# Kernel tuning notes

Hardware: AMD Instinct MI355X
Metric: run time of the kernel (lower is better)

## Reference

```python
import jax, jax.numpy as jnp
import numpy as np
import math

NHID = 8; NHEADS = 8; ALPHA = 0.2; EMB = 64  # nhid*nheads must equal selfattention embed_dim=64
NPROT = 2048; NDRUG = 1500; FPROT = 512; FDRUG = 256; NPAIR = 16384


def _layernorm(x, g, b):
    m = x.mean(-1, keepdims=True)
    v = ((x - m) ** 2).mean(-1, keepdims=True)
    return (x - m) / jnp.sqrt(v + 1e-5) * g + b


def _gat(h, adj, W, a):
    # W: [H,F,O], a: [H,2O].  e_ij = leakyrelu(Wh_i . a1 + Wh_j . a2)
    # (equivalent to the repeat_interleave/repeat/cat construction in the torch code)
    Wh = jnp.einsum('nf,hfo->hno', h, W)                 # [H,N,O]
    s1 = jnp.einsum('hno,ho->hn', Wh, a[:, :NHID])       # [H,N]
    s2 = jnp.einsum('hno,ho->hn', Wh, a[:, NHID:])       # [H,N]
    e = s1[:, :, None] + s2[:, None, :]                  # [H,N,N]
    e = jnp.where(e > 0, e, ALPHA * e)                   # LeakyReLU(alpha)
    e = jnp.where(adj[None, :, :] > 0, e, jnp.float32(-9e15))
    attn = jax.nn.softmax(e, axis=-1)
    out = jax.nn.relu(jnp.einsum('hnm,hmo->hno', attn, Wh))
    H, N, O = out.shape
    return out.transpose(1, 0, 2).reshape(N, H * O)      # concat heads along dim 1


def _mhsa_sum(x, W, b):
    # Sum of NHEADS independent selfattention(64, NHEADS) modules applied to x[None].
    # x: [N,EMB]; W: [3,M,EMB,EMB] torch (out,in) layout; b: [3,M,EMB]
    M = W.shape[1]; N = x.shape[0]; hd = EMB // NHEADS
    qkv = jnp.einsum('nd,smod->smno', x, W) + b[:, :, None, :]   # [3,M,N,EMB]
    q, k, v = [t.reshape(M, N, NHEADS, hd) for t in (qkv[0], qkv[1], qkv[2])]
    scores = jnp.einsum('mnhd,mkhd->mhnk', q, k) / math.sqrt(hd)
    attn = jax.nn.softmax(scores, axis=-1)
    out = jnp.einsum('mhnk,mkhd->mnhd', attn, v).reshape(M, N, EMB)
    return out.sum(0)


def _branch(h, adj, g1W, g1a, p1W, s1W, s1b, l1g, l1b, g2W, g2a, p2W, s2W, s2b, l2g, l2b):
    x = _gat(h, adj, g1W, g1a) @ p1W.T
    x = _layernorm(_mhsa_sum(x, s1W, s1b) + x, l1g, l1b)
    x = _gat(x, adj, g2W, g2a) @ p2W.T
    x = _layernorm(_mhsa_sum(x, s2W, s2b) + x, l2g, l2b)
    return x


def _forward(fl, idx):
    (pf, padj, df, dadj,
     pg1W, pg1a, pp1W, ps1W, ps1b, pl1g, pl1b, pg2W, pg2a, pp2W, ps2W, ps2b, pl2g, pl2b,
     dg1W, dg1a, dp1W, ds1W, ds1b, dl1g, dl1b, dg2W, dg2a, dp2W, ds2W, ds2b, dl2g, dl2b,
     fc1W, fc1b, fc2W, fc2b, fc3W, fc3b) = fl
    px = _branch(pf, padj, pg1W, pg1a, pp1W, ps1W, ps1b, pl1g, pl1b, pg2W, pg2a, pp2W, ps2W, ps2b, pl2g, pl2b)
    dx = _branch(df, dadj, dg1W, dg1a, dp1W, ds1W, ds1b, dl1g, dl1b, dg2W, dg2a, dp2W, ds2W, ds2b, dl2g, dl2b)
    x = jnp.concatenate([px[idx[:, 0]], dx[idx[:, 1]]], axis=1)   # [B, 2*EMB]
    x = jax.nn.relu(x @ fc1W.T + fc1b)
    x = jax.nn.relu(x @ fc2W.T + fc2b)
    return (x @ fc3W.T + fc3b)[:, 0]


def setup_inputs() -> dict:
    key = jax.random.key(0)
    ks = iter(jax.random.split(key, 80))
    nk = lambda: next(ks)
    rn = lambda shape, s=0.1: jax.random.normal(nk(), shape, jnp.float32) * s

    def adj(n):
        a = (jax.random.uniform(nk(), (n, n)) < 0.05).astype(jnp.float32)
        return jnp.maximum(a, jnp.eye(n, dtype=jnp.float32))

    inp = {}
    inp['protein_features'] = rn((NPROT, FPROT), 1.0)
    inp['protein_adj'] = adj(NPROT)
    inp['drug_features'] = rn((NDRUG, FDRUG), 1.0)
    inp['drug_adj'] = adj(NDRUG)
    ip = jax.random.randint(nk(), (NPAIR,), 0, NPROT)
    idd = jax.random.randint(nk(), (NPAIR,), 0, NDRUG)
    inp['idx_protein_drug'] = jnp.stack([ip, idd], axis=1).astype(jnp.int32)
    for pref, F in (('p', FPROT), ('d', FDRUG)):
        inp[pref + '_gat1_W'] = rn((NHEADS, F, NHID))
        inp[pref + '_gat1_a'] = rn((NHEADS, 2 * NHID))
        inp[pref + '_pro1_W'] = rn((EMB, EMB))
        inp[pref + '_sa1_W'] = rn((3, NHEADS, EMB, EMB))
        inp[pref + '_sa1_b'] = jnp.zeros((3, NHEADS, EMB), jnp.float32)
        inp[pref + '_ln1_g'] = jnp.ones((EMB,), jnp.float32)
        inp[pref + '_ln1_b'] = jnp.zeros((EMB,), jnp.float32)
        inp[pref + '_gat2_W'] = rn((NHEADS, EMB, NHID))
        inp[pref + '_gat2_a'] = rn((NHEADS, 2 * NHID))
        inp[pref + '_pro2_W'] = rn((EMB, EMB))
        inp[pref + '_sa2_W'] = rn((3, NHEADS, EMB, EMB))
        inp[pref + '_sa2_b'] = jnp.zeros((3, NHEADS, EMB), jnp.float32)
        inp[pref + '_ln2_g'] = jnp.ones((EMB,), jnp.float32)
        inp[pref + '_ln2_b'] = jnp.zeros((EMB,), jnp.float32)
    inp['fc1_W'] = rn((2 * EMB, 2 * EMB)); inp['fc1_b'] = jnp.zeros((2 * EMB,), jnp.float32)
    inp['fc2_W'] = rn((2 * EMB, 2 * EMB)); inp['fc2_b'] = jnp.zeros((2 * EMB,), jnp.float32)
    inp['fc3_W'] = rn((1, 2 * EMB)); inp['fc3_b'] = jnp.zeros((1,), jnp.float32)
    return inp


def reference(protein_features, protein_adj, drug_features, drug_adj, idx_protein_drug,
              p_gat1_W, p_gat1_a, p_pro1_W, p_sa1_W, p_sa1_b, p_ln1_g, p_ln1_b,
              p_gat2_W, p_gat2_a, p_pro2_W, p_sa2_W, p_sa2_b, p_ln2_g, p_ln2_b,
              d_gat1_W, d_gat1_a, d_pro1_W, d_sa1_W, d_sa1_b, d_ln1_g, d_ln1_b,
              d_gat2_W, d_gat2_a, d_pro2_W, d_sa2_W, d_sa2_b, d_ln2_g, d_ln2_b,
              fc1_W, fc1_b, fc2_W, fc2_b, fc3_W, fc3_b):
    fl = (protein_features, protein_adj, drug_features, drug_adj,
          p_gat1_W, p_gat1_a, p_pro1_W, p_sa1_W, p_sa1_b, p_ln1_g, p_ln1_b,
          p_gat2_W, p_gat2_a, p_pro2_W, p_sa2_W, p_sa2_b, p_ln2_g, p_ln2_b,
          d_gat1_W, d_gat1_a, d_pro1_W, d_sa1_W, d_sa1_b, d_ln1_g, d_ln1_b,
          d_gat2_W, d_gat2_a, d_pro2_W, d_sa2_W, d_sa2_b, d_ln2_g, d_ln2_b,
          fc1_W, fc1_b, fc2_W, fc2_b, fc3_W, fc3_b)
    return _forward(fl, idx_protein_drug)
```

## Files before the change

### kernel.cpp

```cpp
#include <hip/hip_runtime.h>
#include <math.h>

#define NHID 8
#define NHEADS 8
#define EMB 64
#define NPROT 2048
#define NDRUG 1500
#define NPAIR 16384

__global__ void k_gat_wh(const float* __restrict__ h, const float* __restrict__ W,
                         float* __restrict__ Wh, int N, int F) {
    int idx = blockIdx.x * 256 + threadIdx.x;
    int total = NHEADS * N * NHID;
    if (idx >= total) return;
    int o  = idx & 7;
    int n  = (idx >> 3) % N;
    int hh = idx / (N * 8);
    const float* hp = h + (size_t)n * F;
    const float* wp = W + (size_t)hh * F * 8 + o;
    float acc = 0.f;
    for (int f = 0; f < F; ++f) acc += hp[f] * wp[(size_t)f * 8];
    Wh[idx] = acc;
}

__global__ void k_gat_s(const float* __restrict__ Wh, const float* __restrict__ a,
                        float* __restrict__ s1, float* __restrict__ s2, int N) {
    int idx = blockIdx.x * 256 + threadIdx.x;
    if (idx >= NHEADS * N) return;
    int hh = idx / N;
    const float* wp = Wh + (size_t)idx * 8;
    const float* ap = a + hh * 16;
    float x1 = 0.f, x2 = 0.f;
    for (int o = 0; o < 8; ++o) { x1 += wp[o] * ap[o]; x2 += wp[o] * ap[8 + o]; }
    s1[idx] = x1; s2[idx] = x2;
}

__global__ void k_gat_attn(const float* __restrict__ adj, const float* __restrict__ s1,
                           const float* __restrict__ s2, const float* __restrict__ Wh,
                           float* __restrict__ out, int N) {
    __shared__ int nbr[2048];
    __shared__ int s_cnt;
    int i = blockIdx.x;
    int tid = threadIdx.x;
    if (tid == 0) s_cnt = 0;
    __syncthreads();
    const float* arow = adj + (size_t)i * N;
    for (int j = tid; j < N; j += 256)
        if (arow[j] > 0.f) { int p = atomicAdd(&s_cnt, 1); nbr[p] = j; }
    __syncthreads();
    int cnt = s_cnt;
    int g  = tid >> 5;
    int ln = tid & 31;
    float si = s1[g * N + i];
    const float* s2h = s2 + g * N;
    float mx = -1e30f;
    for (int t = ln; t < cnt; t += 32) {
        float e = si + s2h[nbr[t]];
        e = e > 0.f ? e : 0.2f * e;
        mx = fmaxf(mx, e);
    }
    #pragma unroll
    for (int off = 16; off; off >>= 1) mx = fmaxf(mx, __shfl_xor(mx, off, 32));
    float acc[8] = {0, 0, 0, 0, 0, 0, 0, 0};
    float lsum = 0.f;
    for (int t = ln; t < cnt; t += 32) {
        int j = nbr[t];
        float e = si + s2h[j];
        e = e > 0.f ? e : 0.2f * e;
        float p = __expf(e - mx);
        lsum += p;
        const float4* wp = (const float4*)(Wh + ((size_t)g * N + j) * 8);
        float4 w0 = wp[0], w1 = wp[1];
        acc[0] += p * w0.x; acc[1] += p * w0.y; acc[2] += p * w0.z; acc[3] += p * w0.w;
        acc[4] += p * w1.x; acc[5] += p * w1.y; acc[6] += p * w1.z; acc[7] += p * w1.w;
    }
    #pragma unroll
    for (int off = 16; off; off >>= 1) {
        lsum += __shfl_xor(lsum, off, 32);
        #pragma unroll
        for (int d = 0; d < 8; ++d) acc[d] += __shfl_xor(acc[d], off, 32);
    }
    if (ln == 0) {
        float inv = 1.f / lsum;
        #pragma unroll
        for (int d = 0; d < 8; ++d) {
            float r = acc[d] * inv;
            out[(size_t)i * 64 + g * 8 + d] = r > 0.f ? r : 0.f;
        }
    }
}

__global__ void k_proj(const float* __restrict__ in, const float* __restrict__ W,
                       float* __restrict__ out, int N) {
    int idx = blockIdx.x * 256 + threadIdx.x;
    if (idx >= N * 64) return;
    int o = idx & 63, n = idx >> 6;
    const float* ip = in + (size_t)n * 64;
    const float* wp = W + (size_t)o * 64;
    float acc = 0.f;
    for (int d = 0; d < 64; ++d) acc += ip[d] * wp[d];
    out[idx] = acc;
}

__global__ void k_qkv(const float* __restrict__ x, const float* __restrict__ W,
                      const float* __restrict__ b, float* __restrict__ qkv, int N) {
    int idx = blockIdx.x * 256 + threadIdx.x;
    int total = 24 * N * 64;
    if (idx >= total) return;
    int o = idx & 63;
    int n = (idx >> 6) % N;
    int sm = idx / (N * 64);
    const float* xp = x + (size_t)n * 64;
    const float* wp = W + ((size_t)sm * 64 + o) * 64;
    float acc = b[sm * 64 + o];
    for (int d = 0; d < 64; ++d) acc += xp[d] * wp[d];
    qkv[(size_t)sm * N * 64 + (size_t)(o >> 3) * N * 8 + (size_t)n * 8 + (o & 7)] = acc;
}

#define QLOAD(qa, qb, r) { int row_ = row0 + (r); if (row_ >= N) row_ = 0;        \
    const float4* qp_ = (const float4*)(qsl + (size_t)row_ * 8);                  \
    qa = qp_[0]; qb = qp_[1];                                                     \
    qa.x *= qs; qa.y *= qs; qa.z *= qs; qa.w *= qs;                               \
    qb.x *= qs; qb.y *= qs; qb.z *= qs; qb.w *= qs; }

#define ROWSTEP(qa, qb, ca, cb, lr) {                                             \
    float s_ = fmaf(qa.x, kk0.x, fmaf(qa.y, kk0.y, fmaf(qa.z, kk0.z,              \
               fmaf(qa.w, kk0.w, fmaf(qb.x, kk1.x, fmaf(qb.y, kk1.y,              \
               fmaf(qb.z, kk1.z, qb.w * kk1.w)))))));                             \
    float p_ = exp2f(s_); lr += p_;                                               \
    ca.x = fmaf(p_, vv0.x, ca.x); ca.y = fmaf(p_, vv0.y, ca.y);                   \
    ca.z = fmaf(p_, vv0.z, ca.z); ca.w = fmaf(p_, vv0.w, ca.w);                   \
    cb.x = fmaf(p_, vv1.x, cb.x); cb.y = fmaf(p_, vv1.y, cb.y);                   \
    cb.z = fmaf(p_, vv1.z, cb.z); cb.w = fmaf(p_, vv1.w, cb.w); }

#define BF3A(v) { v += __shfl_xor(v, 1, 64); v += __shfl_xor(v, 2, 64);           \
                  v += __shfl_xor(v, 4, 64); }

#define ROWOUT(ca, cb, lr, r) {                                                   \
    BF3A(ca.x); BF3A(ca.y); BF3A(ca.z); BF3A(ca.w);                               \
    BF3A(cb.x); BF3A(cb.y); BF3A(cb.z); BF3A(cb.w); BF3A(lr);                     \
    int sel_ = ln & 7;                                                            \
    float t_ = (sel_ == 0) ? ca.x : (sel_ == 1) ? ca.y : (sel_ == 2) ? ca.z :     \
               (sel_ == 3) ? ca.w : (sel_ == 4) ? cb.x : (sel_ == 5) ? cb.y :     \
               (sel_ == 6) ? cb.z : cb.w;                                         \
    t_ += __shfl_xor(t_, 8, 64); t_ += __shfl_xor(t_, 16, 64);                    \
    t_ += __shfl_xor(t_, 32, 64);                                                 \
    lr += __shfl_xor(lr, 8, 64); lr += __shfl_xor(lr, 16, 64);                    \
    lr += __shfl_xor(lr, 32, 64);                                                 \
    int row_ = row0 + (r);                                                        \
    if (ln < 8 && row_ < N)                                                       \
        atomicAdd(&accum[(size_t)row_ * 64 + hh * 8 + ln], t_ / (lr - phantom)); }

__global__ __launch_bounds__(256, 2)
void k_attn(const float* __restrict__ qkv, float* __restrict__ accum, int N) {
    __shared__ float4 kvt[256];
    int bid = blockIdx.x;
    int m  = bid & 7;
    int hh = (bid >> 3) & 7;
    int rt = bid >> 6;
    int wid = threadIdx.x >> 6, ln = threadIdx.x & 63;
    int row0 = rt * 32 + wid * 8;
    const float* qsl = qkv + (size_t)m        * N * 64 + (size_t)hh * N * 8;
    const float* ksl = qkv + (size_t)(8 + m)  * N * 64 + (size_t)hh * N * 8;
    const float* vsl = qkv + (size_t)(16 + m) * N * 64 + (size_t)hh * N * 8;

    const float qs = 0.35355339059327373f * 1.44269504088896341f;
    float4 q0a, q0b, q1a, q1b, q2a, q2b, q3a, q3b;
    float4 q4a, q4b, q5a, q5b, q6a, q6b, q7a, q7b;
    QLOAD(q0a, q0b, 0) QLOAD(q1a, q1b, 1) QLOAD(q2a, q2b, 2) QLOAD(q3a, q3b, 3)
    QLOAD(q4a, q4b, 4) QLOAD(q5a, q5b, 5) QLOAD(q6a, q6b, 6) QLOAD(q7a, q7b, 7)

    int sj = threadIdx.x >> 2;
    int part = threadIdx.x & 3;
    const float* sb = (part < 2) ? ksl : vsl;
    int halfo = (part & 1) * 4;
    float4* wdst = &kvt[sj * 4 + (part ^ ((sj >> 1) & 3))];

    int Tt = (N + 63) >> 6;
    float4 pre = (sj < N) ? *(const float4*)(sb + (size_t)sj * 8 + halfo)
                          : make_float4(0.f, 0.f, 0.f, 0.f);

    float l0 = 0.f, l1 = 0.f, l2 = 0.f, l3 = 0.f, l4 = 0.f, l5 = 0.f, l6 = 0.f, l7 = 0.f;
    float4 z4 = make_float4(0.f, 0.f, 0.f, 0.f);
    float4 c0a = z4, c0b = z4, c1a = z4, c1b = z4, c2a = z4, c2b = z4, c3a = z4, c3b = z4;
    float4 c4a = z4, c4b = z4, c5a = z4, c5b = z4, c6a = z4, c6b = z4, c7a = z4, c7b = z4;

    int sw = (ln >> 1) & 3;
    const float4* rbase = &kvt[ln * 4];

    for (int t = 0; t < Tt; ++t) {
        __syncthreads();
        *wdst = pre;
        __syncthreads();
        if (t + 1 < Tt) {
            int j = (t + 1) * 64 + sj;
            pre = (j < N) ? *(const float4*)(sb + (size_t)j * 8 + halfo)
                          : make_float4(0.f, 0.f, 0.f, 0.f);
        }
        float4 kk0 = rbase[0 ^ sw], kk1 = rbase[1 ^ sw];
        float4 vv0 = rbase[2 ^ sw], vv1 = rbase[3 ^ sw];
        ROWSTEP(q0a, q0b, c0a, c0b, l0) ROWSTEP(q1a, q1b, c1a, c1b, l1)
        ROWSTEP(q2a, q2b, c2a, c2b, l2) ROWSTEP(q3a, q3b, c3a, c3b, l3)
        ROWSTEP(q4a, q4b, c4a, c4b, l4) ROWSTEP(q5a, q5b, c5a, c5b, l5)
        ROWSTEP(q6a, q6b, c6a, c6b, l6) ROWSTEP(q7a, q7b, c7a, c7b, l7)
    }

    float phantom = (float)(Tt * 64 - N);
    ROWOUT(c0a, c0b, l0, 0) ROWOUT(c1a, c1b, l1, 1)
    ROWOUT(c2a, c2b, l2, 2) ROWOUT(c3a, c3b, l3, 3)
    ROWOUT(c4a, c4b, l4, 4) ROWOUT(c5a, c5b, l5, 5)
    ROWOUT(c6a, c6b, l6, 6) ROWOUT(c7a, c7b, l7, 7)
}

__global__ void k_ln(const float* __restrict__ acc, const float* __restrict__ resid,
                     const float* __restrict__ g, const float* __restrict__ b,
                     float* __restrict__ out, int N) {
    int r = blockIdx.x * 4 + (threadIdx.x >> 6);
    int d = threadIdx.x & 63;
    if (r >= N) return;
    float v = acc[(size_t)r * 64 + d] + resid[(size_t)r * 64 + d];
    float s = v;
    for (int off = 32; off; off >>= 1) s += __shfl_xor(s, off, 64);
    float mean = s * (1.f / 64.f);
    float c = v - mean;
    float vv = c * c;
    for (int off = 32; off; off >>= 1) vv += __shfl_xor(vv, off, 64);
    float var = vv * (1.f / 64.f);
    out[(size_t)r * 64 + d] = c * rsqrtf(var + 1e-5f) * g[d] + b[d];
}

#define MLP_STEP(ai, xi) {                                                        \
    ai.x = fmaf(xi.x, w0.x, fmaf(xi.y, w0.y, fmaf(xi.z, w0.z, fmaf(xi.w, w0.w, ai.x)))); \
    ai.y = fmaf(xi.x, w1.x, fmaf(xi.y, w1.y, fmaf(xi.z, w1.z, fmaf(xi.w, w1.w, ai.y)))); \
    ai.z = fmaf(xi.x, w2.x, fmaf(xi.y, w2.y, fmaf(xi.z, w2.z, fmaf(xi.w, w2.w, ai.z)))); \
    ai.w = fmaf(xi.x, w3.x, fmaf(xi.y, w3.y, fmaf(xi.z, w3.z, fmaf(xi.w, w3.w, ai.w)))); }

#define MLP_LAYER(B_)                                                             \
    a0 = z4; a1 = z4; a2 = z4; a3 = z4; a4 = z4; a5 = z4; a6 = z4; a7 = z4;       \
    _Pragma("unroll 4")                                                           \
    for (int k4 = 0; k4 < 32; ++k4) {                                             \
        float4 w0 = sW4[og][k4 ^ swz];                                            \
        float4 w1 = sW4[og + 32][k4 ^ swz];                                       \
        float4 w2 = sW4[og + 64][k4 ^ swz];                                       \
        float4 w3 = sW4[og + 96][k4 ^ swz];                                       \
        float4 x0 = sX4[pb + 0][k4], x1 = sX4[pb + 1][k4];                        \
        float4 x2 = sX4[pb + 2][k4], x3 = sX4[pb + 3][k4];                        \
        float4 x4 = sX4[pb + 4][k4], x5 = sX4[pb + 5][k4];                        \
        float4 x6 = sX4[pb + 6][k4], x7 = sX4[pb + 7][k4];                        \
        MLP_STEP(a0, x0) MLP_STEP(a1, x1) MLP_STEP(a2, x2) MLP_STEP(a3, x3)       \
        MLP_STEP(a4, x4) MLP_STEP(a5, x5) MLP_STEP(a6, x6) MLP_STEP(a7, x7)       \
    }                                                                             \
    {                                                                             \
        float bo0 = B_[og], bo1 = B_[og + 32], bo2 = B_[og + 64], bo3 = B_[og + 96]; \
        a0.x += bo0; a0.y += bo1; a0.z += bo2; a0.w += bo3;                       \
        a1.x += bo0; a1.y += bo1; a1.z += bo2; a1.w += bo3;                       \
        a2.x += bo0; a2.y += bo1; a2.z += bo2; a2.w += bo3;                       \
        a3.x += bo0; a3.y += bo1; a3.z += bo2; a3.w += bo3;                       \
        a4.x += bo0; a4.y += bo1; a4.z += bo2; a4.w += bo3;                       \
        a5.x += bo0; a5.y += bo1; a5.z += bo2; a5.w += bo3;                       \
        a6.x += bo0; a6.y += bo1; a6.z += bo2; a6.w += bo3;                       \
        a7.x += bo0; a7.y += bo1; a7.z += bo2; a7.w += bo3;                       \
    }

#define MLP_HWRITE(ai, i) {                                                       \
    float* hp_ = sXf + (size_t)(pb + (i)) * 128;                                  \
    hp_[og]      = ai.x > 0.f ? ai.x : 0.f;                                       \
    hp_[og + 32] = ai.y > 0.f ? ai.y : 0.f;                                       \
    hp_[og + 64] = ai.z > 0.f ? ai.z : 0.f;                                       \
    hp_[og + 96] = ai.w > 0.f ? ai.w : 0.f; }

#define MLP_WLOAD(Wg_) {                                                          \
    const float4* wsrc_ = (const float4*)(Wg_);                                   \
    _Pragma("unroll")                                                             \
    for (int u = 0; u < 16; ++u) {                                                \
        int f4 = u * 256 + t;                                                     \
        int o_ = f4 >> 5, k4_ = f4 & 31;                                          \
        sW4[o_][k4_ ^ (o_ & 7)] = wsrc_[f4];                                      \
    } }

__global__ __launch_bounds__(256, 1)
void k_mlp(const float* __restrict__ px, const float* __restrict__ dx,
           const int* __restrict__ pairs,
           const float* __restrict__ W1, const float* __restrict__ b1,
           const float* __restrict__ W2, const float* __restrict__ b2,
           const float* __restrict__ W3, const float* __restrict__ b3,
           float* __restrict__ out) {
    __shared__ float4 sX4[64][32];
    __shared__ float4 sW4[128][32];
    float* sXf = (float*)sX4;
    int t = threadIdx.x;
    int base = blockIdx.x * 64;

    #pragma unroll
    for (int u = 0; u < 8; ++u) {
        int idx = u * 256 + t;
        int p = idx >> 5, c4 = idx & 31;
        int ip = pairs[(base + p) * 2], id = pairs[(base + p) * 2 + 1];
        float4 v = (c4 < 16) ? ((const float4*)px)[(size_t)ip * 16 + c4]
                             : ((const float4*)dx)[(size_t)id * 16 + (c4 - 16)];
        sX4[p][c4] = v;
    }
    MLP_WLOAD(W1)
    __syncthreads();

    int og = t & 31;
    int pb = (t >> 5) * 8;
    int swz = og & 7;
    float4 z4 = make_float4(0.f, 0.f, 0.f, 0.f);
    float4 a0, a1, a2, a3, a4, a5, a6, a7;

    MLP_LAYER(b1)
    __syncthreads();
    MLP_HWRITE(a0, 0) MLP_HWRITE(a1, 1) MLP_HWRITE(a2, 2) MLP_HWRITE(a3, 3)
    MLP_HWRITE(a4, 4) MLP_HWRITE(a5, 5) MLP_HWRITE(a6, 6) MLP_HWRITE(a7, 7)
    MLP_WLOAD(W2)
    __syncthreads();

    MLP_LAYER(b2)
    __syncthreads();
    MLP_HWRITE(a0, 0) MLP_HWRITE(a1, 1) MLP_HWRITE(a2, 2) MLP_HWRITE(a3, 3)
    MLP_HWRITE(a4, 4) MLP_HWRITE(a5, 5) MLP_HWRITE(a6, 6) MLP_HWRITE(a7, 7)
    __syncthreads();

    {
        int p = t >> 2, qd = t & 3;
        const float4* w3 = (const float4*)W3;
        float sum = 0.f;
        #pragma unroll
        for (int u = 0; u < 8; ++u) {
            float4 h = sX4[p][qd * 8 + u];
            float4 w = w3[qd * 8 + u];
            sum += h.x * w.x + h.y * w.y + h.z * w.z + h.w * w.w;
        }
        sum += __shfl_xor(sum, 1, 64);
        sum += __shfl_xor(sum, 2, 64);
        if ((t & 3) == 0) out[base + p] = sum + b3[0];
    }
}

extern "C" void kernel_launch(void* const* d_in, const int* in_sizes, int n_in,
                              void* d_out, int out_size, void* d_ws, size_t ws_size,
                              hipStream_t stream) {
    const float* pfeat = (const float*)d_in[0];
    const float* padj  = (const float*)d_in[1];
    const float* dfeat = (const float*)d_in[2];
    const float* dadj  = (const float*)d_in[3];
    const int*   pairs = (const int*)d_in[4];
    const float* fc1W = (const float*)d_in[33];
    const float* fc1b = (const float*)d_in[34];
    const float* fc2W = (const float*)d_in[35];
    const float* fc2b = (const float*)d_in[36];
    const float* fc3W = (const float*)d_in[37];
    const float* fc3b = (const float*)d_in[38];

    float* ws = (float*)d_ws;
    float* buf_Wh   = ws;
    float* buf_s1   = buf_Wh   + 8 * 2048 * 8;
    float* buf_s2   = buf_s1   + 8 * 2048;
    float* buf_gat  = buf_s2   + 8 * 2048;
    float* buf_proj = buf_gat  + 2048 * 64;
    float* buf_qkv  = buf_proj + 2048 * 64;
    float* buf_acc  = buf_qkv  + 24 * 2048 * 64;
    float* buf_x    = buf_acc  + 2048 * 64;
    float* buf_px   = buf_x    + 2048 * 64;
    float* buf_dx   = buf_px   + 2048 * 64;

    auto run_branch = [&](const float* feat, const float* adj, int N, int F,
                          void* const* w, float* xout) {
        const float* g1W = (const float*)w[0];
        const float* g1a = (const float*)w[1];
        const float* p1W = (const float*)w[2];
        const float* s1W = (const float*)w[3];
        const float* s1b = (const float*)w[4];
        const float* l1g = (const float*)w[5];
        const float* l1b = (const float*)w[6];
        const float* g2W = (const float*)w[7];
        const float* g2a = (const float*)w[8];
        const float* p2W = (const float*)w[9];
        const float* s2W = (const float*)w[10];
        const float* s2b = (const float*)w[11];
        const float* l2g = (const float*)w[12];
        const float* l2b = (const float*)w[13];

        int attnGrid = 64 * ((N + 31) / 32);

        k_gat_wh<<<(64 * N + 255) / 256, 256, 0, stream>>>(feat, g1W, buf_Wh, N, F);
        k_gat_s<<<(8 * N + 255) / 256, 256, 0, stream>>>(buf_Wh, g1a, buf_s1, buf_s2, N);
        k_gat_attn<<<N, 256, 0, stream>>>(adj, buf_s1, buf_s2, buf_Wh, buf_gat, N);
        k_proj<<<(64 * N + 255) / 256, 256, 0, stream>>>(buf_gat, p1W, buf_proj, N);
        k_qkv<<<(1536 * N + 255) / 256, 256, 0, stream>>>(buf_proj, s1W, s1b, buf_qkv, N);
        hipMemsetAsync(buf_acc, 0, (size_t)N * 64 * sizeof(float), stream);
        k_attn<<<attnGrid, 256, 0, stream>>>(buf_qkv, buf_acc, N);
        k_ln<<<(N + 3) / 4, 256, 0, stream>>>(buf_acc, buf_proj, l1g, l1b, buf_x, N);
        k_gat_wh<<<(64 * N + 255) / 256, 256, 0, stream>>>(buf_x, g2W, buf_Wh, N, EMB);
        k_gat_s<<<(8 * N + 255) / 256, 256, 0, stream>>>(buf_Wh, g2a, buf_s1, buf_s2, N);
        k_gat_attn<<<N, 256, 0, stream>>>(adj, buf_s1, buf_s2, buf_Wh, buf_gat, N);
        k_proj<<<(64 * N + 255) / 256, 256, 0, stream>>>(buf_gat, p2W, buf_proj, N);
        k_qkv<<<(1536 * N + 255) / 256, 256, 0, stream>>>(buf_proj, s2W, s2b, buf_qkv, N);
        hipMemsetAsync(buf_acc, 0, (size_t)N * 64 * sizeof(float), stream);
        k_attn<<<attnGrid, 256, 0, stream>>>(buf_qkv, buf_acc, N);
        k_ln<<<(N + 3) / 4, 256, 0, stream>>>(buf_acc, buf_proj, l2g, l2b, xout, N);
    };

    run_branch(pfeat, padj, NPROT, 512, d_in + 5, buf_px);
    run_branch(dfeat, dadj, NDRUG, 256, d_in + 19, buf_dx);

    k_mlp<<<NPAIR / 64, 256, 0, stream>>>(buf_px, buf_dx, pairs,
                                          fc1W, fc1b, fc2W, fc2b, fc3W, fc3b,
                                          (float*)d_out);
}
```

Before: 1.391 ms.

## Use fp16 dot2 for attention scores and vectorize GAT/QKV loads

Keys and pre-scaled queries in the self-attention kernel are converted to fp16 so each score is computed with packed fdot2 instructions. K is stored packed in LDS, which changes the shared-memory slot layout. The occupancy hint rises from 2 to 3 blocks per SIMD, and the GAT Wh and QKV projection kernels switch to float4 loads with fused multiply-adds. The aim is fewer ALU ops and lower register pressure in the hot attention loop, at the cost of fp16 rounding in the attention scores.

```diff
diff --git a/kernel.cpp b/kernel.cpp
--- a/kernel.cpp
+++ b/kernel.cpp
@@ -7,6 +7,8 @@
 #define NPROT 2048
 #define NDRUG 1500
 #define NPAIR 16384
+
+typedef _Float16 h2 __attribute__((ext_vector_type(2)));
 
 __global__ void k_gat_wh(const float* __restrict__ h, const float* __restrict__ W,
                          float* __restrict__ Wh, int N, int F) {
@@ -16,10 +18,15 @@
     int o  = idx & 7;
     int n  = (idx >> 3) % N;
     int hh = idx / (N * 8);
-    const float* hp = h + (size_t)n * F;
+    const float4* hp4 = (const float4*)(h + (size_t)n * F);
     const float* wp = W + (size_t)hh * F * 8 + o;
     float acc = 0.f;
-    for (int f = 0; f < F; ++f) acc += hp[f] * wp[(size_t)f * 8];
+    for (int f4 = 0; f4 < (F >> 2); ++f4) {
+        float4 hv = hp4[f4];
+        int fb = f4 * 32;
+        acc = fmaf(hv.x, wp[fb], fmaf(hv.y, wp[fb + 8],
+              fmaf(hv.z, wp[fb + 16], fmaf(hv.w, wp[fb + 24], acc))));
+    }
     Wh[idx] = acc;
 }
 
@@ -110,23 +117,30 @@
     int o = idx & 63;
     int n = (idx >> 6) % N;
     int sm = idx / (N * 64);
-    const float* xp = x + (size_t)n * 64;
-    const float* wp = W + ((size_t)sm * 64 + o) * 64;
+    const float4* xp4 = (const float4*)(x + (size_t)n * 64);
+    const float4* wp4 = (const float4*)(W + ((size_t)sm * 64 + o) * 64);
     float acc = b[sm * 64 + o];
-    for (int d = 0; d < 64; ++d) acc += xp[d] * wp[d];
+    #pragma unroll 4
+    for (int d4 = 0; d4 < 16; ++d4) {
+        float4 xv = xp4[d4], wv = wp4[d4];
+        acc = fmaf(xv.x, wv.x, fmaf(xv.y, wv.y, fmaf(xv.z, wv.z, fmaf(xv.w, wv.w, acc))));
+    }
     qkv[(size_t)sm * N * 64 + (size_t)(o >> 3) * N * 8 + (size_t)n * 8 + (o & 7)] = acc;
 }
 
-#define QLOAD(qa, qb, r) { int row_ = row0 + (r); if (row_ >= N) row_ = 0;        \
+#define QLOADH(qa, qb, qc, qd, r) { int row_ = row0 + (r); if (row_ >= N) row_ = 0; \
     const float4* qp_ = (const float4*)(qsl + (size_t)row_ * 8);                  \
-    qa = qp_[0]; qb = qp_[1];                                                     \
-    qa.x *= qs; qa.y *= qs; qa.z *= qs; qa.w *= qs;                               \
-    qb.x *= qs; qb.y *= qs; qb.z *= qs; qb.w *= qs; }
-
-#define ROWSTEP(qa, qb, ca, cb, lr) {                                             \
-    float s_ = fmaf(qa.x, kk0.x, fmaf(qa.y, kk0.y, fmaf(qa.z, kk0.z,              \
-               fmaf(qa.w, kk0.w, fmaf(qb.x, kk1.x, fmaf(qb.y, kk1.y,              \
-               fmaf(qb.z, kk1.z, qb.w * kk1.w)))))));                             \
+    float4 a_ = qp_[0], b_ = qp_[1];                                              \
+    qa = h2{(_Float16)(a_.x * qs), (_Float16)(a_.y * qs)};                        \
+    qb = h2{(_Float16)(a_.z * qs), (_Float16)(a_.w * qs)};                        \
+    qc = h2{(_Float16)(b_.x * qs), (_Float16)(b_.y * qs)};                        \
+    qd = h2{(_Float16)(b_.z * qs), (_Float16)(b_.w * qs)}; }
+
+#define ROWSTEPH(qa, qb, qc, qd, ca, cb, lr) {                                    \
+    float s_ = __builtin_amdgcn_fdot2(qa, kk0,                                    \
+               __builtin_amdgcn_fdot2(qb, kk1,                                    \
+               __builtin_amdgcn_fdot2(qc, kk2,                                    \
+               __builtin_amdgcn_fdot2(qd, kk3, 0.f, false), false), false), false);\
     float p_ = exp2f(s_); lr += p_;                                               \
     ca.x = fmaf(p_, vv0.x, ca.x); ca.y = fmaf(p_, vv0.y, ca.y);                   \
     ca.z = fmaf(p_, vv0.z, ca.z); ca.w = fmaf(p_, vv0.w, ca.w);                   \
@@ -151,7 +165,7 @@
     if (ln < 8 && row_ < N)                                                       \
         atomicAdd(&accum[(size_t)row_ * 64 + hh * 8 + ln], t_ / (lr - phantom)); }
 
-__global__ __launch_bounds__(256, 2)
+__global__ __launch_bounds__(256, 3)
 void k_attn(const float* __restrict__ qkv, float* __restrict__ accum, int N) {
     __shared__ float4 kvt[256];
     int bid = blockIdx.x;
@@ -165,16 +179,22 @@
     const float* vsl = qkv + (size_t)(16 + m) * N * 64 + (size_t)hh * N * 8;
 
     const float qs = 0.35355339059327373f * 1.44269504088896341f;
-    float4 q0a, q0b, q1a, q1b, q2a, q2b, q3a, q3b;
-    float4 q4a, q4b, q5a, q5b, q6a, q6b, q7a, q7b;
-    QLOAD(q0a, q0b, 0) QLOAD(q1a, q1b, 1) QLOAD(q2a, q2b, 2) QLOAD(q3a, q3b, 3)
-    QLOAD(q4a, q4b, 4) QLOAD(q5a, q5b, 5) QLOAD(q6a, q6b, 6) QLOAD(q7a, q7b, 7)
+    h2 q0a, q0b, q0c, q0d, q1a, q1b, q1c, q1d, q2a, q2b, q2c, q2d, q3a, q3b, q3c, q3d;
+    h2 q4a, q4b, q4c, q4d, q5a, q5b, q5c, q5d, q6a, q6b, q6c, q6d, q7a, q7b, q7c, q7d;
+    QLOADH(q0a, q0b, q0c, q0d, 0) QLOADH(q1a, q1b, q1c, q1d, 1)
+    QLOADH(q2a, q2b, q2c, q2d, 2) QLOADH(q3a, q3b, q3c, q3d, 3)
+    QLOADH(q4a, q4b, q4c, q4d, 4) QLOADH(q5a, q5b, q5c, q5d, 5)
+    QLOADH(q6a, q6b, q6c, q6d, 6) QLOADH(q7a, q7b, q7c, q7d, 7)
 
     int sj = threadIdx.x >> 2;
     int part = threadIdx.x & 3;
-    const float* sb = (part < 2) ? ksl : vsl;
-    int halfo = (part & 1) * 4;
-    float4* wdst = &kvt[sj * 4 + (part ^ ((sj >> 1) & 3))];
+    bool isK = (part == 0) | (part == 3);
+    const float* sb = isK ? ksl : vsl;
+    int halfo = (part & 2) ? 4 : 0;
+    int slot_base = isK ? 0 : (part == 1 ? 1 : 2);
+    int slot = slot_base ^ ((sj >> 1) & 3);
+    float4* vdst = &kvt[sj * 4 + slot];
+    float2* kdst = (float2*)((char*)&kvt[sj * 4 + slot] + ((part == 3) ? 8 : 0));
 
     int Tt = (N + 63) >> 6;
     float4 pre = (sj < N) ? *(const float4*)(sb + (size_t)sj * 8 + halfo)
@@ -190,19 +210,36 @@
 
     for (int t = 0; t < Tt; ++t) {
         __syncthreads();
-        *wdst = pre;
+        if (isK) {
+            h2 lo = h2{(_Float16)pre.x, (_Float16)pre.y};
+            h2 hi = h2{(_Float16)pre.z, (_Float16)pre.w};
+            float2 st;
+            st.x = __builtin_bit_cast(float, lo);
+            st.y = __builtin_bit_cast(float, hi);
+            *kdst = st;
+        } else {
+            *vdst = pre;
+        }
         __syncthreads();
         if (t + 1 < Tt) {
             int j = (t + 1) * 64 + sj;
             pre = (j < N) ? *(const float4*)(sb + (size_t)j * 8 + halfo)
                           : make_float4(0.f, 0.f, 0.f, 0.f);
         }
-        float4 kk0 = rbase[0 ^ sw], kk1 = rbase[1 ^ sw];
-        float4 vv0 = rbase[2 ^ sw], vv1 = rbase[3 ^ sw];
-        ROWSTEP(q0a, q0b, c0a, c0b, l0) ROWSTEP(q1a, q1b, c1a, c1b, l1)
-        ROWSTEP(q2a, q2b, c2a, c2b, l2) ROWSTEP(q3a, q3b, c3a, c3b, l3)
-        ROWSTEP(q4a, q4b, c4a, c4b, l4) ROWSTEP(q5a, q5b, c5a, c5b, l5)
-        ROWSTEP(q6a, q6b, c6a, c6b, l6) ROWSTEP(q7a, q7b, c7a, c7b, l7)
+        float4 kf = rbase[0 ^ sw];
+        h2 kk0 = __builtin_bit_cast(h2, kf.x);
+        h2 kk1 = __builtin_bit_cast(h2, kf.y);
+        h2 kk2 = __builtin_bit_cast(h2, kf.z);
+        h2 kk3 = __builtin_bit_cast(h2, kf.w);
+        float4 vv0 = rbase[1 ^ sw], vv1 = rbase[2 ^ sw];
+        ROWSTEPH(q0a, q0b, q0c, q0d, c0a, c0b, l0)
+        ROWSTEPH(q1a, q1b, q1c, q1d, c1a, c1b, l1)
+        ROWSTEPH(q2a, q2b, q2c, q2d, c2a, c2b, l2)
+        ROWSTEPH(q3a, q3b, q3c, q3d, c3a, c3b, l3)
+        ROWSTEPH(q4a, q4b, q4c, q4d, c4a, c4b, l4)
+        ROWSTEPH(q5a, q5b, q5c, q5d, c5a, c5b, l5)
+        ROWSTEPH(q6a, q6b, q6c, q6d, c6a, c6b, l6)
+        ROWSTEPH(q7a, q7b, q7c, q7d, c7a, c7b, l7)
     }
 
     float phantom = (float)(Tt * 64 - N);
```

Result: faster. 1.274 ms (-8.4%).
